# Kernel tuning notes

Hardware: AMD Instinct MI355X
Metric: run time of the kernel (lower is better)

Reference implementation:

```python
import math
import jax, jax.numpy as jnp
import numpy as np

B, T, D = 2048, 50, 256
NEG = -100000.0

def setup_inputs() -> dict:
    key = jax.random.key(0)
    ks = jax.random.split(key, 9)
    return {
        "x": jax.random.normal(ks[0], (B, T, D), dtype=jnp.float32),
        "mask": jax.random.randint(ks[1], (B, T, 1), 0, 2, dtype=jnp.int32),
        "time_decay": jax.random.uniform(ks[2], (B, T, 1), dtype=jnp.float32),
        "Wq": jax.random.normal(ks[3], (D, D), dtype=jnp.float32) * (1.0 / math.sqrt(D)),
        "bq": jax.random.normal(ks[4], (D,), dtype=jnp.float32) * 0.01,
        "Wk": jax.random.normal(ks[5], (D, D), dtype=jnp.float32) * (1.0 / math.sqrt(D)),
        "bk": jax.random.normal(ks[6], (D,), dtype=jnp.float32) * 0.01,
        "Wv": jax.random.normal(ks[7], (D, D), dtype=jnp.float32) * (1.0 / math.sqrt(D)),
        "bv": jax.random.normal(ks[8], (D,), dtype=jnp.float32) * 0.01,
    }

def reference(x, mask, time_decay, Wq, bq, Wk, bk, Wv, bv):
    # PositionalEncoding.forward: elementwise multiply by time-decay (broadcast over d_model)
    x = x * time_decay  # [B,T,D]
    q = jnp.einsum('btd,ed->bte', x, Wq) + bq
    k = jnp.einsum('btd,ed->bte', x, Wk) + bk
    v = jnp.einsum('btd,ed->bte', x, Wv) + bv
    # unusual Q/K-side masking (masked_fill before the matmul)
    keep = mask != 0  # [B,T,1]
    q = jnp.where(keep, q, NEG)
    k = jnp.where(keep, k, NEG)
    score = jnp.einsum('btd,bsd->bts', q, k) / math.sqrt(D)  # [B,T,T]
    score = jax.nn.softmax(score, axis=-1)
    # dropout is identity in eval mode
    out = jnp.einsum('bts,bsd->btd', score, v)  # [B,T,D]
    return out[:, -1, :]  # [B,D]
```

## Files before the change

kernel.cpp:

```cpp
#include <hip/hip_runtime.h>


namespace {
constexpr int kB = 2048;
constexpr int kT = 50;
constexpr int kD = 256;
constexpr int kBB = 4;
constexpr double kNeg = -100000.0;
constexpr int oM2 = 0;
constexpr int oWvp = 65536;
constexpr int oV0 = 131072;
constexpr int oC = 131328;
constexpr int oW1 = 131584;
constexpr int oW2 = 131840;
constexpr int oDbl = 132096;
}

__global__ __launch_bounds__(256) void precomp(
    const float* __restrict__ Wq, const float* __restrict__ bq,
    const float* __restrict__ Wk, const float* __restrict__ bk,
    const float* __restrict__ Wv, float* __restrict__ ws) {
  const int t = threadIdx.x;
  const int wave = t >> 6;
  const int lane = t & 63;
  const int blk = blockIdx.x;
  __shared__ float coefL[kD];
  __shared__ double red[3][4];

  if (blk < 256) {
    const int a = blk;
    coefL[t] = Wq[(size_t)t * kD + a];
    __syncthreads();
    const float* kcol = Wk + t;
    float pre[8];
#pragma unroll
    for (int k = 0; k < 8; ++k) pre[k] = kcol[(size_t)k * kD];
    float acc = 0.f;
    for (int j0 = 0; j0 < kD; j0 += 8) {
      float cur[8];
#pragma unroll
      for (int k = 0; k < 8; ++k) cur[k] = pre[k];
      const int nx = (j0 + 8 < kD) ? (j0 + 8) : 0;
#pragma unroll
      for (int k = 0; k < 8; ++k) pre[k] = kcol[(size_t)(nx + k) * kD];
#pragma unroll
      for (int k = 0; k < 8; ++k) acc += coefL[j0 + k] * cur[k];
    }
    ws[oM2 + (a >> 2) * 1024 + 4 * t + (a & 3)] = acc;
  } else if (blk < 258) {
    const float* W = (blk == 256) ? Wk : Wq;
    const float* coef = (blk == 256) ? bq : bk;
    coefL[t] = coef[t];
    __syncthreads();
    const float* col = W + t;
    float pre[8];
#pragma unroll
    for (int k = 0; k < 8; ++k) pre[k] = col[(size_t)k * kD];
    double a0 = 0.0, a1 = 0.0;
    for (int j0 = 0; j0 < kD; j0 += 8) {
      float cur[8];
#pragma unroll
      for (int k = 0; k < 8; ++k) cur[k] = pre[k];
      const int nx = (j0 + 8 < kD) ? (j0 + 8) : 0;
#pragma unroll
      for (int k = 0; k < 8; ++k) pre[k] = col[(size_t)(nx + k) * kD];
#pragma unroll
      for (int k = 0; k < 8; ++k) {
        const double w = (double)cur[k];
        a0 += (double)coefL[j0 + k] * w;
        a1 += w;
      }
    }
    if (blk == 256) {
      ws[oV0 + t] = (float)a0;
      ws[oC + t] = (float)a1;
    } else {
      ws[oW1 + t] = (float)a0;
      ws[oW2 + t] = (float)a1;
      double p0 = (double)bk[t];
      double p1 = (double)bq[t] * (double)bk[t];
      double p2 = (double)bq[t];
#pragma unroll
      for (int off = 32; off; off >>= 1) {
        p0 += __shfl_xor(p0, off);
        p1 += __shfl_xor(p1, off);
        p2 += __shfl_xor(p2, off);
      }
      if (lane == 0) {
        red[0][wave] = p0;
        red[1][wave] = p1;
        red[2][wave] = p2;
      }
      __syncthreads();
      if (t == 0) {
        double* dcw = (double*)(ws + oDbl);
        dcw[0] = red[0][0] + red[0][1] + red[0][2] + red[0][3];
        dcw[1] = red[1][0] + red[1][1] + red[1][2] + red[1][3];
        dcw[2] = red[2][0] + red[2][1] + red[2][2] + red[2][3];
      }
    }
  } else {
    const int d4b = (blk - 258) * 4;
    float4 in[4];
#pragma unroll
    for (int k = 0; k < 4; ++k)
      in[k] = *(const float4*)(Wv + (size_t)t * kD + 4 * (d4b + k));
    float4* Wvp = (float4*)(ws + oWvp);
#pragma unroll
    for (int k = 0; k < 4; ++k) Wvp[(size_t)(d4b + k) * kD + t] = in[k];
  }
}

__global__ __launch_bounds__(512) void fused_main(
    const float* __restrict__ x, const int* __restrict__ mask,
    const float* __restrict__ td, const float* __restrict__ bv,
    const float* __restrict__ ws, float* __restrict__ out) {
  const int tid = threadIdx.x;
  const int lane = tid & 63;
  const int w = tid >> 6;
  const int b0 = blockIdx.x * kBB;
  __shared__ __align__(16) float xsL[kBB][kD];
  __shared__ __align__(16) float uL[kBB][kD];
  __shared__ __align__(16) float yL[kBB][kD];
  __shared__ __align__(16) float scr[2][kBB][kD];
  __shared__ double mpart[kBB][2];
  __shared__ float lpart[kBB][2];
  __shared__ double dScal[kBB][2];

  const double* dc = (const double*)(ws + oDbl);
  const float4* M2v = (const float4*)(ws + oM2);
  const float4* Wvv = (const float4*)(ws + oWvp);

  const int ja = w >> 1;
  const int h = w & 1;
  const float mtdA = (lane < kT) ? td[(size_t)(b0 + ja) * kT + lane] : 0.f;
  const int mmkA = (lane < kT) ? mask[(size_t)(b0 + ja) * kT + lane] : 0;
  const float4 c4 = ((const float4*)(ws + oC))[lane];

  if (w < kBB) {
    const int j = w;
    const int b = b0 + j;
    const float tdl = td[(size_t)b * kT + kT - 1];
    const float4 a1 = ((const float4*)(ws + oW1))[lane];
    const float4 a2 = ((const float4*)(ws + oW2))[lane];
    const float4 xv =
        ((const float4*)(x + ((size_t)b * kT + kT - 1) * kD))[lane];
    double s1 = (double)xv.x * a1.x + (double)xv.y * a1.y +
                (double)xv.z * a1.z + (double)xv.w * a1.w;
    double s2 = (double)xv.x * a2.x + (double)xv.y * a2.y +
                (double)xv.z * a2.z + (double)xv.w * a2.w;
#pragma unroll
    for (int off = 32; off; off >>= 1) {
      s1 += __shfl_xor(s1, off);
      s2 += __shfl_xor(s2, off);
    }
    if (lane == 0) {
      dScal[j][0] = (double)tdl * s1 + dc[1];
      dScal[j][1] = (double)tdl * s2 + dc[2];
    }
    float4 xs;
    xs.x = xv.x * tdl; xs.y = xv.y * tdl;
    xs.z = xv.z * tdl; xs.w = xv.w * tdl;
    *(float4*)(&xsL[j][4 * lane]) = xs;
  }
  __syncthreads();

  {
    const int gU = w & 3;
    const int kh = w >> 2;
    const int col = 64 * gU + lane;
    const int kb = kh * 32;
    float4 A = M2v[(size_t)(kb + 0) * 256 + col];
    float4 B = M2v[(size_t)(kb + 1) * 256 + col];
    float4 C = M2v[(size_t)(kb + 2) * 256 + col];
    float4 D = M2v[(size_t)(kb + 3) * 256 + col];
    float acc[kBB] = {0.f, 0.f, 0.f, 0.f};
    for (int k4 = kb; k4 < kb + 32; k4 += 2) {
      const float4 c0 = A, c1 = B;
      A = C;
      B = D;
      const int n0 = (k4 + 4 < kb + 32) ? k4 + 4 : kb;
      const int n1 = (k4 + 5 < kb + 32) ? k4 + 5 : kb;
      C = M2v[(size_t)n0 * 256 + col];
      D = M2v[(size_t)n1 * 256 + col];
#pragma unroll
      for (int jb = 0; jb < kBB; ++jb) {
        const float4 x0 = *(const float4*)(&xsL[jb][4 * k4]);
        const float4 x1 = *(const float4*)(&xsL[jb][4 * (k4 + 1)]);
        acc[jb] += x0.x * c0.x + x0.y * c0.y + x0.z * c0.z + x0.w * c0.w +
                   x1.x * c1.x + x1.y * c1.y + x1.z * c1.z + x1.w * c1.w;
      }
    }
#pragma unroll
    for (int jb = 0; jb < kBB; ++jb) scr[kh][jb][col] = acc[jb];
  }
  __syncthreads();

  {
#pragma unroll
    for (int rr = 0; rr < 2; ++rr) {
      const int idx = tid + rr * 512;
      const int mj = idx >> 8;
      const int mcol = idx & 255;
      uL[mj][mcol] = scr[0][mj][mcol] + scr[1][mj][mcol] + ws[oV0 + mcol];
    }
  }
  __syncthreads();

  {
    const int j = ja;
    const int b = b0 + j;
    const float mtd = mtdA;
    const int mmk = mmkA;
    const int mqg = __shfl(mmk, kT - 1);
    const float4 u4 = *(const float4*)(&uL[j][4 * lane]);
    const float4 v4 = mqg ? u4 : c4;
    const double Qb = dScal[j][0];
    const double Cm = kNeg * dScal[j][1] * 0.0625;
    const double sbkd = dc[0];
    const double Cbb = 256.0 * 1.0e10 * 0.0625;
    const int sbeg = h ? 24 : 0;
    const int send = h ? 50 : 24;

    const float4* xrow = (const float4*)(x + (size_t)b * kT * kD);
    double m = -1.0e300;
    float l = 0.f;
    float4 y = {0.f, 0.f, 0.f, 0.f};

    float4 n0 = xrow[(size_t)(sbeg + 0) * 64 + lane];
    float4 n1 = xrow[(size_t)(sbeg + 1) * 64 + lane];
    float4 n2 = xrow[(size_t)(sbeg + 2) * 64 + lane];
    float4 n3 = xrow[(size_t)(sbeg + 3) * 64 + lane];
    for (int s = sbeg; s < send; s += 4) {
      const float4 r0 = n0, r1 = n1, r2 = n2, r3 = n3;
      {
        const int p0 = (s + 4 < kT) ? s + 4 : kT - 1;
        const int p1 = (s + 5 < kT) ? s + 5 : kT - 1;
        const int p2 = (s + 6 < kT) ? s + 6 : kT - 1;
        const int p3 = (s + 7 < kT) ? s + 7 : kT - 1;
        n0 = xrow[(size_t)p0 * 64 + lane];
        n1 = xrow[(size_t)p1 * 64 + lane];
        n2 = xrow[(size_t)p2 * 64 + lane];
        n3 = xrow[(size_t)p3 * 64 + lane];
      }
      const int s1i = s + 1, s2i = s + 2, s3i = s + 3;
      const int cc0 = s;
      const int cc1 = (s1i < kT) ? s1i : kT - 1;
      const int cc2 = (s2i < kT) ? s2i : kT - 1;
      const int cc3 = (s3i < kT) ? s3i : kT - 1;
      const float tv0 = __shfl(mtd, cc0);
      const float tv1 = __shfl(mtd, cc1);
      const float tv2 = __shfl(mtd, cc2);
      const float tv3 = __shfl(mtd, cc3);
      float4 a0, aa1, a2v, a3;
      a0.x = r0.x * tv0; a0.y = r0.y * tv0; a0.z = r0.z * tv0; a0.w = r0.w * tv0;
      aa1.x = r1.x * tv1; aa1.y = r1.y * tv1; aa1.z = r1.z * tv1; aa1.w = r1.w * tv1;
      a2v.x = r2.x * tv2; a2v.y = r2.y * tv2; a2v.z = r2.z * tv2; a2v.w = r2.w * tv2;
      a3.x = r3.x * tv3; a3.y = r3.y * tv3; a3.z = r3.z * tv3; a3.w = r3.w * tv3;
      float p0 = a0.x * v4.x + a0.y * v4.y + a0.z * v4.z + a0.w * v4.w;
      float p1 = aa1.x * v4.x + aa1.y * v4.y + aa1.z * v4.z + aa1.w * v4.w;
      float p2 = a2v.x * v4.x + a2v.y * v4.y + a2v.z * v4.z + a2v.w * v4.w;
      float p3 = a3.x * v4.x + a3.y * v4.y + a3.z * v4.z + a3.w * v4.w;
#pragma unroll
      for (int off = 32; off; off >>= 1) {
        p0 += __shfl_xor(p0, off);
        p1 += __shfl_xor(p1, off);
        p2 += __shfl_xor(p2, off);
        p3 += __shfl_xor(p3, off);
      }
      const int ms0 = __shfl(mmk, cc0);
      const int ms1 = __shfl(mmk, cc1);
      const int ms2 = __shfl(mmk, cc2);
      const int ms3 = __shfl(mmk, cc3);
      double sc0, sc1, sc2, sc3;
      if (mqg) {
        sc0 = ms0 ? ((double)p0 + Qb) * 0.0625 : Cm;
        sc1 = ms1 ? ((double)p1 + Qb) * 0.0625 : Cm;
        sc2 = ms2 ? ((double)p2 + Qb) * 0.0625 : Cm;
        sc3 = ms3 ? ((double)p3 + Qb) * 0.0625 : Cm;
      } else {
        sc0 = ms0 ? kNeg * ((double)p0 + sbkd) * 0.0625 : Cbb;
        sc1 = ms1 ? kNeg * ((double)p1 + sbkd) * 0.0625 : Cbb;
        sc2 = ms2 ? kNeg * ((double)p2 + sbkd) * 0.0625 : Cbb;
        sc3 = ms3 ? kNeg * ((double)p3 + sbkd) * 0.0625 : Cbb;
      }
      if (s1i >= send) sc1 = -1.0e300;
      if (s2i >= send) sc2 = -1.0e300;
      if (s3i >= send) sc3 = -1.0e300;
      double mnew = m;
      if (sc0 > mnew) mnew = sc0;
      if (sc1 > mnew) mnew = sc1;
      if (sc2 > mnew) mnew = sc2;
      if (sc3 > mnew) mnew = sc3;
      const float al = __expf((float)(m - mnew));
      const float e0 = __expf((float)(sc0 - mnew));
      const float e1 = __expf((float)(sc1 - mnew));
      const float e2 = __expf((float)(sc2 - mnew));
      const float e3 = __expf((float)(sc3 - mnew));
      m = mnew;
      l = l * al + e0 + e1 + e2 + e3;
      y.x = y.x * al + e0 * a0.x + e1 * aa1.x + e2 * a2v.x + e3 * a3.x;
      y.y = y.y * al + e0 * a0.y + e1 * aa1.y + e2 * a2v.y + e3 * a3.y;
      y.z = y.z * al + e0 * a0.z + e1 * aa1.z + e2 * a2v.z + e3 * a3.z;
      y.w = y.w * al + e0 * a0.w + e1 * aa1.w + e2 * a2v.w + e3 * a3.w;
    }
    if (lane == 0) {
      mpart[j][h] = m;
      lpart[j][h] = l;
    }
    *(float4*)(&scr[h][j][4 * lane]) = y;
  }
  __syncthreads();

  {
    float yv[2];
    int mjA[2], mcolA[2];
#pragma unroll
    for (int rr = 0; rr < 2; ++rr) {
      const int idx = tid + rr * 512;
      const int mj = idx >> 8;
      const int mcol = idx & 255;
      const double m0 = mpart[mj][0], m1 = mpart[mj][1];
      const double M = (m0 > m1) ? m0 : m1;
      const float e0 = __expf((float)(m0 - M));
      const float e1 = __expf((float)(m1 - M));
      const float l = lpart[mj][0] * e0 + lpart[mj][1] * e1;
      yv[rr] = (scr[0][mj][mcol] * e0 + scr[1][mj][mcol] * e1) * (1.0f / l);
      mjA[rr] = mj;
      mcolA[rr] = mcol;
    }
    __syncthreads();
    yL[mjA[0]][mcolA[0]] = yv[0];
    yL[mjA[1]][mcolA[1]] = yv[1];
  }
  __syncthreads();

  {
    const int gU = w & 3;
    const int kh = w >> 2;
    const int col = 64 * gU + lane;
    const int kb = kh * 32;
    float4 A = Wvv[(size_t)(kb + 0) * 256 + col];
    float4 B = Wvv[(size_t)(kb + 1) * 256 + col];
    float4 C = Wvv[(size_t)(kb + 2) * 256 + col];
    float4 D = Wvv[(size_t)(kb + 3) * 256 + col];
    float acc[kBB] = {0.f, 0.f, 0.f, 0.f};
    for (int k4 = kb; k4 < kb + 32; k4 += 2) {
      const float4 c0 = A, c1 = B;
      A = C;
      B = D;
      const int n0 = (k4 + 4 < kb + 32) ? k4 + 4 : kb;
      const int n1 = (k4 + 5 < kb + 32) ? k4 + 5 : kb;
      C = Wvv[(size_t)n0 * 256 + col];
      D = Wvv[(size_t)n1 * 256 + col];
#pragma unroll
      for (int jb = 0; jb < kBB; ++jb) {
        const float4 y0 = *(const float4*)(&yL[jb][4 * k4]);
        const float4 y1 = *(const float4*)(&yL[jb][4 * (k4 + 1)]);
        acc[jb] += y0.x * c0.x + y0.y * c0.y + y0.z * c0.z + y0.w * c0.w +
                   y1.x * c1.x + y1.y * c1.y + y1.z * c1.z + y1.w * c1.w;
      }
    }
#pragma unroll
    for (int jb = 0; jb < kBB; ++jb) scr[kh][jb][col] = acc[jb];
  }
  __syncthreads();

  {
#pragma unroll
    for (int rr = 0; rr < 2; ++rr) {
      const int idx = tid + rr * 512;
      const int mj = idx >> 8;
      const int mcol = idx & 255;
      out[(size_t)(b0 + mj) * kD + mcol] =
          scr[0][mj][mcol] + scr[1][mj][mcol] + bv[mcol];
    }
  }
}

extern "C" void kernel_launch(void* const* d_in, const int* in_sizes, int n_in,
                              void* d_out, int out_size, void* d_ws,
                              size_t ws_size, hipStream_t stream) {
  const float* x = (const float*)d_in[0];
  const int* mask = (const int*)d_in[1];
  const float* td = (const float*)d_in[2];
  const float* Wq = (const float*)d_in[3];
  const float* bq = (const float*)d_in[4];
  const float* Wk = (const float*)d_in[5];
  const float* bk = (const float*)d_in[6];
  const float* Wv = (const float*)d_in[7];
  const float* bv = (const float*)d_in[8];
  float* ws = (float*)d_ws;
  float* out = (float*)d_out;
  (void)in_sizes; (void)n_in; (void)out_size; (void)ws_size;

  hipLaunchKernelGGL(precomp, dim3(274), dim3(256), 0, stream, Wq, bq, Wk, bk,
                     Wv, ws);
  hipLaunchKernelGGL(fused_main, dim3(kB / kBB), dim3(512), 0, stream, x, mask,
                     td, bv, (const float*)ws, out);
}
```

Before: 202.0 us.

## Split fused kernel into u-projection, per-batch attention, and output projection kernels

Breaks the single fused kernel into three launches: a batched GEMV computing u into the output buffer, an attention kernel with one block per batch row that splits the 50 keys across four waves, and a batched Wv projection kernel. The aim is more blocks and more waves per batch row in the bandwidth-heavy attention stage, which streams x, so that stage gets better parallelism. In exchange it adds two extra kernel launches and a round trip of the intermediates through global memory via the output buffer.

```diff
diff --git a/kernel.cpp b/kernel.cpp
--- a/kernel.cpp
+++ b/kernel.cpp
@@ -5,7 +5,6 @@
 constexpr int kB = 2048;
 constexpr int kT = 50;
 constexpr int kD = 256;
-constexpr int kBB = 4;
 constexpr double kNeg = -100000.0;
 constexpr int oM2 = 0;
 constexpr int oWvp = 65536;
@@ -111,57 +110,26 @@
   }
 }
 
-__global__ __launch_bounds__(512) void fused_main(
-    const float* __restrict__ x, const int* __restrict__ mask,
-    const float* __restrict__ td, const float* __restrict__ bv,
-    const float* __restrict__ ws, float* __restrict__ out) {
+__global__ __launch_bounds__(512) void ukernel(
+    const float* __restrict__ x, const float* __restrict__ td,
+    const float* __restrict__ ws, float* __restrict__ uout) {
   const int tid = threadIdx.x;
   const int lane = tid & 63;
   const int w = tid >> 6;
-  const int b0 = blockIdx.x * kBB;
-  __shared__ __align__(16) float xsL[kBB][kD];
-  __shared__ __align__(16) float uL[kBB][kD];
-  __shared__ __align__(16) float yL[kBB][kD];
-  __shared__ __align__(16) float scr[2][kBB][kD];
-  __shared__ double mpart[kBB][2];
-  __shared__ float lpart[kBB][2];
-  __shared__ double dScal[kBB][2];
-
-  const double* dc = (const double*)(ws + oDbl);
+  const int b0 = blockIdx.x * 4;
+  __shared__ __align__(16) float xsL[4][kD];
+  __shared__ __align__(16) float scr[2][4][kD];
   const float4* M2v = (const float4*)(ws + oM2);
-  const float4* Wvv = (const float4*)(ws + oWvp);
-
-  const int ja = w >> 1;
-  const int h = w & 1;
-  const float mtdA = (lane < kT) ? td[(size_t)(b0 + ja) * kT + lane] : 0.f;
-  const int mmkA = (lane < kT) ? mask[(size_t)(b0 + ja) * kT + lane] : 0;
-  const float4 c4 = ((const float4*)(ws + oC))[lane];
-
-  if (w < kBB) {
-    const int j = w;
-    const int b = b0 + j;
+
+  if (w < 4) {
+    const int b = b0 + w;
     const float tdl = td[(size_t)b * kT + kT - 1];
-    const float4 a1 = ((const float4*)(ws + oW1))[lane];
-    const float4 a2 = ((const float4*)(ws + oW2))[lane];
     const float4 xv =
         ((const float4*)(x + ((size_t)b * kT + kT - 1) * kD))[lane];
-    double s1 = (double)xv.x * a1.x + (double)xv.y * a1.y +
-                (double)xv.z * a1.z + (double)xv.w * a1.w;
-    double s2 = (double)xv.x * a2.x + (double)xv.y * a2.y +
-                (double)xv.z * a2.z + (double)xv.w * a2.w;
-#pragma unroll
-    for (int off = 32; off; off >>= 1) {
-      s1 += __shfl_xor(s1, off);
-      s2 += __shfl_xor(s2, off);
-    }
-    if (lane == 0) {
-      dScal[j][0] = (double)tdl * s1 + dc[1];
-      dScal[j][1] = (double)tdl * s2 + dc[2];
-    }
     float4 xs;
     xs.x = xv.x * tdl; xs.y = xv.y * tdl;
     xs.z = xv.z * tdl; xs.w = xv.w * tdl;
-    *(float4*)(&xsL[j][4 * lane]) = xs;
+    *(float4*)(&xsL[w][4 * lane]) = xs;
   }
   __syncthreads();
 
@@ -174,7 +142,7 @@
     float4 B = M2v[(size_t)(kb + 1) * 256 + col];
     float4 C = M2v[(size_t)(kb + 2) * 256 + col];
     float4 D = M2v[(size_t)(kb + 3) * 256 + col];
-    float acc[kBB] = {0.f, 0.f, 0.f, 0.f};
+    float acc[4] = {0.f, 0.f, 0.f, 0.f};
     for (int k4 = kb; k4 < kb + 32; k4 += 2) {
       const float4 c0 = A, c1 = B;
       A = C;
@@ -184,7 +152,7 @@
       C = M2v[(size_t)n0 * 256 + col];
       D = M2v[(size_t)n1 * 256 + col];
 #pragma unroll
-      for (int jb = 0; jb < kBB; ++jb) {
+      for (int jb = 0; jb < 4; ++jb) {
         const float4 x0 = *(const float4*)(&xsL[jb][4 * k4]);
         const float4 x1 = *(const float4*)(&xsL[jb][4 * (k4 + 1)]);
         acc[jb] += x0.x * c0.x + x0.y * c0.y + x0.z * c0.z + x0.w * c0.w +
@@ -192,146 +160,193 @@
       }
     }
 #pragma unroll
-    for (int jb = 0; jb < kBB; ++jb) scr[kh][jb][col] = acc[jb];
+    for (int jb = 0; jb < 4; ++jb) scr[kh][jb][col] = acc[jb];
   }
   __syncthreads();
 
+#pragma unroll
+  for (int rr = 0; rr < 2; ++rr) {
+    const int idx = tid + rr * 512;
+    const int mj = idx >> 8;
+    const int mcol = idx & 255;
+    uout[(size_t)(b0 + mj) * kD + mcol] =
+        scr[0][mj][mcol] + scr[1][mj][mcol] + ws[oV0 + mcol];
+  }
+}
+
+__global__ __launch_bounds__(256) void attnk(
+    const float* __restrict__ x, const int* __restrict__ mask,
+    const float* __restrict__ td, const float* __restrict__ ws,
+    float* __restrict__ uy) {
+  const int tid = threadIdx.x;
+  const int lane = tid & 63;
+  const int q = tid >> 6;
+  const int b = blockIdx.x;
+  __shared__ __align__(16) float ypart[4][kD];
+  __shared__ double mpart[4];
+  __shared__ float lpart[4];
+
+  const double* dc = (const double*)(ws + oDbl);
+
+  const float mtd = (lane < kT) ? td[(size_t)b * kT + lane] : 0.f;
+  const int mmk = (lane < kT) ? mask[(size_t)b * kT + lane] : 0;
+  const float4 c4 = ((const float4*)(ws + oC))[lane];
+  const float4 u4 = ((const float4*)(uy + (size_t)b * kD))[lane];
+
+  const float tdl = __shfl(mtd, kT - 1);
+  const float4 a1 = ((const float4*)(ws + oW1))[lane];
+  const float4 a2 = ((const float4*)(ws + oW2))[lane];
+  const float4 xv = ((const float4*)(x + ((size_t)b * kT + kT - 1) * kD))[lane];
+  double s1 = (double)xv.x * a1.x + (double)xv.y * a1.y +
+              (double)xv.z * a1.z + (double)xv.w * a1.w;
+  double s2 = (double)xv.x * a2.x + (double)xv.y * a2.y +
+              (double)xv.z * a2.z + (double)xv.w * a2.w;
+#pragma unroll
+  for (int off = 32; off; off >>= 1) {
+    s1 += __shfl_xor(s1, off);
+    s2 += __shfl_xor(s2, off);
+  }
+  const double Qb = (double)tdl * s1 + dc[1];
+  const double Sq = (double)tdl * s2 + dc[2];
+  const int mqg = __shfl(mmk, kT - 1);
+  const float4 v4 = mqg ? u4 : c4;
+  const double Cm = kNeg * Sq * 0.0625;
+  const double sbkd = dc[0];
+  const double Cbb = 256.0 * 1.0e10 * 0.0625;
+
+  const int sbeg = (q == 0) ? 0 : (q == 1) ? 13 : (q == 2) ? 26 : 38;
+  const int send = (q == 0) ? 13 : (q == 1) ? 26 : (q == 2) ? 38 : 50;
+
+  const float4* xrow = (const float4*)(x + (size_t)b * kT * kD);
+  double m = -1.0e300;
+  float l = 0.f;
+  float4 y = {0.f, 0.f, 0.f, 0.f};
+
+  const int i0 = (sbeg + 0 < kT) ? sbeg + 0 : kT - 1;
+  const int i1 = (sbeg + 1 < kT) ? sbeg + 1 : kT - 1;
+  const int i2 = (sbeg + 2 < kT) ? sbeg + 2 : kT - 1;
+  const int i3 = (sbeg + 3 < kT) ? sbeg + 3 : kT - 1;
+  float4 n0 = xrow[(size_t)i0 * 64 + lane];
+  float4 n1 = xrow[(size_t)i1 * 64 + lane];
+  float4 n2 = xrow[(size_t)i2 * 64 + lane];
+  float4 n3 = xrow[(size_t)i3 * 64 + lane];
+  for (int s = sbeg; s < send; s += 4) {
+    const float4 r0 = n0, r1 = n1, r2 = n2, r3 = n3;
+    {
+      const int p0 = (s + 4 < kT) ? s + 4 : kT - 1;
+      const int p1 = (s + 5 < kT) ? s + 5 : kT - 1;
+      const int p2 = (s + 6 < kT) ? s + 6 : kT - 1;
+      const int p3 = (s + 7 < kT) ? s + 7 : kT - 1;
+      n0 = xrow[(size_t)p0 * 64 + lane];
+      n1 = xrow[(size_t)p1 * 64 + lane];
+      n2 = xrow[(size_t)p2 * 64 + lane];
+      n3 = xrow[(size_t)p3 * 64 + lane];
+    }
+    const int s1i = s + 1, s2i = s + 2, s3i = s + 3;
+    const int cc0 = s;
+    const int cc1 = (s1i < kT) ? s1i : kT - 1;
+    const int cc2 = (s2i < kT) ? s2i : kT - 1;
+    const int cc3 = (s3i < kT) ? s3i : kT - 1;
+    const float tv0 = __shfl(mtd, cc0);
+    const float tv1 = __shfl(mtd, cc1);
+    const float tv2 = __shfl(mtd, cc2);
+    const float tv3 = __shfl(mtd, cc3);
+    float4 a0, aa1, a2v, a3;
+    a0.x = r0.x * tv0; a0.y = r0.y * tv0; a0.z = r0.z * tv0; a0.w = r0.w * tv0;
+    aa1.x = r1.x * tv1; aa1.y = r1.y * tv1; aa1.z = r1.z * tv1; aa1.w = r1.w * tv1;
+    a2v.x = r2.x * tv2; a2v.y = r2.y * tv2; a2v.z = r2.z * tv2; a2v.w = r2.w * tv2;
+    a3.x = r3.x * tv3; a3.y = r3.y * tv3; a3.z = r3.z * tv3; a3.w = r3.w * tv3;
+    float p0 = a0.x * v4.x + a0.y * v4.y + a0.z * v4.z + a0.w * v4.w;
+    float p1 = aa1.x * v4.x + aa1.y * v4.y + aa1.z * v4.z + aa1.w * v4.w;
+    float p2 = a2v.x * v4.x + a2v.y * v4.y + a2v.z * v4.z + a2v.w * v4.w;
+    float p3 = a3.x * v4.x + a3.y * v4.y + a3.z * v4.z + a3.w * v4.w;
+#pragma unroll
+    for (int off = 32; off; off >>= 1) {
+      p0 += __shfl_xor(p0, off);
+      p1 += __shfl_xor(p1, off);
+      p2 += __shfl_xor(p2, off);
+      p3 += __shfl_xor(p3, off);
+    }
+    const int ms0 = __shfl(mmk, cc0);
+    const int ms1 = __shfl(mmk, cc1);
+    const int ms2 = __shfl(mmk, cc2);
+    const int ms3 = __shfl(mmk, cc3);
+    double sc0, sc1, sc2, sc3;
+    if (mqg) {
+      sc0 = ms0 ? ((double)p0 + Qb) * 0.0625 : Cm;
+      sc1 = ms1 ? ((double)p1 + Qb) * 0.0625 : Cm;
+      sc2 = ms2 ? ((double)p2 + Qb) * 0.0625 : Cm;
+      sc3 = ms3 ? ((double)p3 + Qb) * 0.0625 : Cm;
+    } else {
+      sc0 = ms0 ? kNeg * ((double)p0 + sbkd) * 0.0625 : Cbb;
+      sc1 = ms1 ? kNeg * ((double)p1 + sbkd) * 0.0625 : Cbb;
+      sc2 = ms2 ? kNeg * ((double)p2 + sbkd) * 0.0625 : Cbb;
+      sc3 = ms3 ? kNeg * ((double)p3 + sbkd) * 0.0625 : Cbb;
+    }
+    if (s1i >= send) sc1 = -1.0e300;
+    if (s2i >= send) sc2 = -1.0e300;
+    if (s3i >= send) sc3 = -1.0e300;
+    double mnew = m;
+    if (sc0 > mnew) mnew = sc0;
+    if (sc1 > mnew) mnew = sc1;
+    if (sc2 > mnew) mnew = sc2;
+    if (sc3 > mnew) mnew = sc3;
+    const float al = __expf((float)(m - mnew));
+    const float e0 = __expf((float)(sc0 - mnew));
+    const float e1 = __expf((float)(sc1 - mnew));
+    const float e2 = __expf((float)(sc2 - mnew));
+    const float e3 = __expf((float)(sc3 - mnew));
+    m = mnew;
+    l = l * al + e0 + e1 + e2 + e3;
+    y.x = y.x * al + e0 * a0.x + e1 * aa1.x + e2 * a2v.x + e3 * a3.x;
+    y.y = y.y * al + e0 * a0.y + e1 * aa1.y + e2 * a2v.y + e3 * a3.y;
+    y.z = y.z * al + e0 * a0.z + e1 * aa1.z + e2 * a2v.z + e3 * a3.z;
+    y.w = y.w * al + e0 * a0.w + e1 * aa1.w + e2 * a2v.w + e3 * a3.w;
+  }
+  if (lane == 0) {
+    mpart[q] = m;
+    lpart[q] = l;
+  }
+  *(float4*)(&ypart[q][4 * lane]) = y;
+  __syncthreads();
+
   {
-#pragma unroll
-    for (int rr = 0; rr < 2; ++rr) {
-      const int idx = tid + rr * 512;
-      const int mj = idx >> 8;
-      const int mcol = idx & 255;
-      uL[mj][mcol] = scr[0][mj][mcol] + scr[1][mj][mcol] + ws[oV0 + mcol];
-    }
-  }
-  __syncthreads();
-
-  {
-    const int j = ja;
-    const int b = b0 + j;
-    const float mtd = mtdA;
-    const int mmk = mmkA;
-    const int mqg = __shfl(mmk, kT - 1);
-    const float4 u4 = *(const float4*)(&uL[j][4 * lane]);
-    const float4 v4 = mqg ? u4 : c4;
-    const double Qb = dScal[j][0];
-    const double Cm = kNeg * dScal[j][1] * 0.0625;
-    const double sbkd = dc[0];
-    const double Cbb = 256.0 * 1.0e10 * 0.0625;
-    const int sbeg = h ? 24 : 0;
-    const int send = h ? 50 : 24;
-
-    const float4* xrow = (const float4*)(x + (size_t)b * kT * kD);
-    double m = -1.0e300;
-    float l = 0.f;
-    float4 y = {0.f, 0.f, 0.f, 0.f};
-
-    float4 n0 = xrow[(size_t)(sbeg + 0) * 64 + lane];
-    float4 n1 = xrow[(size_t)(sbeg + 1) * 64 + lane];
-    float4 n2 = xrow[(size_t)(sbeg + 2) * 64 + lane];
-    float4 n3 = xrow[(size_t)(sbeg + 3) * 64 + lane];
-    for (int s = sbeg; s < send; s += 4) {
-      const float4 r0 = n0, r1 = n1, r2 = n2, r3 = n3;
-      {
-        const int p0 = (s + 4 < kT) ? s + 4 : kT - 1;
-        const int p1 = (s + 5 < kT) ? s + 5 : kT - 1;
-        const int p2 = (s + 6 < kT) ? s + 6 : kT - 1;
-        const int p3 = (s + 7 < kT) ? s + 7 : kT - 1;
-        n0 = xrow[(size_t)p0 * 64 + lane];
-        n1 = xrow[(size_t)p1 * 64 + lane];
-        n2 = xrow[(size_t)p2 * 64 + lane];
-        n3 = xrow[(size_t)p3 * 64 + lane];
-      }
-      const int s1i = s + 1, s2i = s + 2, s3i = s + 3;
-      const int cc0 = s;
-      const int cc1 = (s1i < kT) ? s1i : kT - 1;
-      const int cc2 = (s2i < kT) ? s2i : kT - 1;
-      const int cc3 = (s3i < kT) ? s3i : kT - 1;
-      const float tv0 = __shfl(mtd, cc0);
-      const float tv1 = __shfl(mtd, cc1);
-      const float tv2 = __shfl(mtd, cc2);
-      const float tv3 = __shfl(mtd, cc3);
-      float4 a0, aa1, a2v, a3;
-      a0.x = r0.x * tv0; a0.y = r0.y * tv0; a0.z = r0.z * tv0; a0.w = r0.w * tv0;
-      aa1.x = r1.x * tv1; aa1.y = r1.y * tv1; aa1.z = r1.z * tv1; aa1.w = r1.w * tv1;
-      a2v.x = r2.x * tv2; a2v.y = r2.y * tv2; a2v.z = r2.z * tv2; a2v.w = r2.w * tv2;
-      a3.x = r3.x * tv3; a3.y = r3.y * tv3; a3.z = r3.z * tv3; a3.w = r3.w * tv3;
-      float p0 = a0.x * v4.x + a0.y * v4.y + a0.z * v4.z + a0.w * v4.w;
-      float p1 = aa1.x * v4.x + aa1.y * v4.y + aa1.z * v4.z + aa1.w * v4.w;
-      float p2 = a2v.x * v4.x + a2v.y * v4.y + a2v.z * v4.z + a2v.w * v4.w;
-      float p3 = a3.x * v4.x + a3.y * v4.y + a3.z * v4.z + a3.w * v4.w;
-#pragma unroll
-      for (int off = 32; off; off >>= 1) {
-        p0 += __shfl_xor(p0, off);
-        p1 += __shfl_xor(p1, off);
-        p2 += __shfl_xor(p2, off);
-        p3 += __shfl_xor(p3, off);
-      }
-      const int ms0 = __shfl(mmk, cc0);
-      const int ms1 = __shfl(mmk, cc1);
-      const int ms2 = __shfl(mmk, cc2);
-      const int ms3 = __shfl(mmk, cc3);
-      double sc0, sc1, sc2, sc3;
-      if (mqg) {
-        sc0 = ms0 ? ((double)p0 + Qb) * 0.0625 : Cm;
-        sc1 = ms1 ? ((double)p1 + Qb) * 0.0625 : Cm;
-        sc2 = ms2 ? ((double)p2 + Qb) * 0.0625 : Cm;
-        sc3 = ms3 ? ((double)p3 + Qb) * 0.0625 : Cm;
-      } else {
-        sc0 = ms0 ? kNeg * ((double)p0 + sbkd) * 0.0625 : Cbb;
-        sc1 = ms1 ? kNeg * ((double)p1 + sbkd) * 0.0625 : Cbb;
-        sc2 = ms2 ? kNeg * ((double)p2 + sbkd) * 0.0625 : Cbb;
-        sc3 = ms3 ? kNeg * ((double)p3 + sbkd) * 0.0625 : Cbb;
-      }
-      if (s1i >= send) sc1 = -1.0e300;
-      if (s2i >= send) sc2 = -1.0e300;
-      if (s3i >= send) sc3 = -1.0e300;
-      double mnew = m;
-      if (sc0 > mnew) mnew = sc0;
-      if (sc1 > mnew) mnew = sc1;
-      if (sc2 > mnew) mnew = sc2;
-      if (sc3 > mnew) mnew = sc3;
-      const float al = __expf((float)(m - mnew));
-      const float e0 = __expf((float)(sc0 - mnew));
-      const float e1 = __expf((float)(sc1 - mnew));
-      const float e2 = __expf((float)(sc2 - mnew));
-      const float e3 = __expf((float)(sc3 - mnew));
-      m = mnew;
-      l = l * al + e0 + e1 + e2 + e3;
-      y.x = y.x * al + e0 * a0.x + e1 * aa1.x + e2 * a2v.x + e3 * a3.x;
-      y.y = y.y * al + e0 * a0.y + e1 * aa1.y + e2 * a2v.y + e3 * a3.y;
-      y.z = y.z * al + e0 * a0.z + e1 * aa1.z + e2 * a2v.z + e3 * a3.z;
-      y.w = y.w * al + e0 * a0.w + e1 * aa1.w + e2 * a2v.w + e3 * a3.w;
-    }
-    if (lane == 0) {
-      mpart[j][h] = m;
-      lpart[j][h] = l;
-    }
-    *(float4*)(&scr[h][j][4 * lane]) = y;
-  }
-  __syncthreads();
-
-  {
-    float yv[2];
-    int mjA[2], mcolA[2];
-#pragma unroll
-    for (int rr = 0; rr < 2; ++rr) {
-      const int idx = tid + rr * 512;
-      const int mj = idx >> 8;
-      const int mcol = idx & 255;
-      const double m0 = mpart[mj][0], m1 = mpart[mj][1];
-      const double M = (m0 > m1) ? m0 : m1;
-      const float e0 = __expf((float)(m0 - M));
-      const float e1 = __expf((float)(m1 - M));
-      const float l = lpart[mj][0] * e0 + lpart[mj][1] * e1;
-      yv[rr] = (scr[0][mj][mcol] * e0 + scr[1][mj][mcol] * e1) * (1.0f / l);
-      mjA[rr] = mj;
-      mcolA[rr] = mcol;
-    }
-    __syncthreads();
-    yL[mjA[0]][mcolA[0]] = yv[0];
-    yL[mjA[1]][mcolA[1]] = yv[1];
+    const int d = tid;
+    double M = mpart[0];
+    if (mpart[1] > M) M = mpart[1];
+    if (mpart[2] > M) M = mpart[2];
+    if (mpart[3] > M) M = mpart[3];
+    const float e0 = __expf((float)(mpart[0] - M));
+    const float e1 = __expf((float)(mpart[1] - M));
+    const float e2 = __expf((float)(mpart[2] - M));
+    const float e3 = __expf((float)(mpart[3] - M));
+    const float lsum = lpart[0] * e0 + lpart[1] * e1 + lpart[2] * e2 +
+                       lpart[3] * e3;
+    const float inv = 1.0f / lsum;
+    uy[(size_t)b * kD + d] =
+        (ypart[0][d] * e0 + ypart[1][d] * e1 + ypart[2][d] * e2 +
+         ypart[3][d] * e3) *
+        inv;
+  }
+}
+
+__global__ __launch_bounds__(512) void okernel(
+    const float* __restrict__ bv, const float* __restrict__ ws,
+    float* __restrict__ io) {
+  const int tid = threadIdx.x;
+  const int lane = tid & 63;
+  const int w = tid >> 6;
+  const int b0 = blockIdx.x * 4;
+  __shared__ __align__(16) float yL[4][kD];
+  __shared__ __align__(16) float scr[2][4][kD];
+  const float4* Wvv = (const float4*)(ws + oWvp);
+
+#pragma unroll
+  for (int rr = 0; rr < 2; ++rr) {
+    const int idx = tid + rr * 512;
+    const int mj = idx >> 8;
+    const int mcol = idx & 255;
+    yL[mj][mcol] = io[(size_t)(b0 + mj) * kD + mcol];
   }
   __syncthreads();
 
@@ -344,7 +359,7 @@
     float4 B = Wvv[(size_t)(kb + 1) * 256 + col];
     float4 C = Wvv[(size_t)(kb + 2) * 256 + col];
     float4 D = Wvv[(size_t)(kb + 3) * 256 + col];
-    float acc[kBB] = {0.f, 0.f, 0.f, 0.f};
+    float acc[4] = {0.f, 0.f, 0.f, 0.f};
     for (int k4 = kb; k4 < kb + 32; k4 += 2) {
       const float4 c0 = A, c1 = B;
       A = C;
@@ -354,7 +369,7 @@
       C = Wvv[(size_t)n0 * 256 + col];
       D = Wvv[(size_t)n1 * 256 + col];
 #pragma unroll
-      for (int jb = 0; jb < kBB; ++jb) {
+      for (int jb = 0; jb < 4; ++jb) {
         const float4 y0 = *(const float4*)(&yL[jb][4 * k4]);
         const float4 y1 = *(const float4*)(&yL[jb][4 * (k4 + 1)]);
         acc[jb] += y0.x * c0.x + y0.y * c0.y + y0.z * c0.z + y0.w * c0.w +
@@ -362,19 +377,17 @@
       }
     }
 #pragma unroll
-    for (int jb = 0; jb < kBB; ++jb) scr[kh][jb][col] = acc[jb];
+    for (int jb = 0; jb < 4; ++jb) scr[kh][jb][col] = acc[jb];
   }
   __syncthreads();
 
-  {
-#pragma unroll
-    for (int rr = 0; rr < 2; ++rr) {
-      const int idx = tid + rr * 512;
-      const int mj = idx >> 8;
-      const int mcol = idx & 255;
-      out[(size_t)(b0 + mj) * kD + mcol] =
-          scr[0][mj][mcol] + scr[1][mj][mcol] + bv[mcol];
-    }
+#pragma unroll
+  for (int rr = 0; rr < 2; ++rr) {
+    const int idx = tid + rr * 512;
+    const int mj = idx >> 8;
+    const int mcol = idx & 255;
+    io[(size_t)(b0 + mj) * kD + mcol] =
+        scr[0][mj][mcol] + scr[1][mj][mcol] + bv[mcol];
   }
 }
 
@@ -396,6 +409,10 @@
 
   hipLaunchKernelGGL(precomp, dim3(274), dim3(256), 0, stream, Wq, bq, Wk, bk,
                      Wv, ws);
-  hipLaunchKernelGGL(fused_main, dim3(kB / kBB), dim3(512), 0, stream, x, mask,
-                     td, bv, (const float*)ws, out);
-}
+  hipLaunchKernelGGL(ukernel, dim3(kB / 4), dim3(512), 0, stream, x, td,
+                     (const float*)ws, out);
+  hipLaunchKernelGGL(attnk, dim3(kB), dim3(256), 0, stream, x, mask, td,
+                     (const float*)ws, out);
+  hipLaunchKernelGGL(okernel, dim3(kB / 4), dim3(512), 0, stream, bv,
+                     (const float*)ws, out);
+}
```

Measured after the change: 206.0 us. About the same (+2.0%).
